# Kernel optimization log

Hardware: AMD Instinct MI355X
Metric: run time of the kernel (lower is better)

## Reference

```python
import jax, jax.numpy as jnp
import numpy as np

EPS = 1e-5
TAU = 2.0

# Heaviside spike with spikingjelly's default Sigmoid surrogate gradient (alpha=4)
@jax.custom_vjp
def spike(x):
    return (x >= 0.0).astype(x.dtype)

def _spike_fwd(x):
    return (x >= 0.0).astype(x.dtype), x

def _spike_bwd(x, g):
    a = 4.0
    s = jax.nn.sigmoid(a * x)
    return (g * a * s * (1.0 - s),)

spike.defvjp(_spike_fwd, _spike_bwd)

def lif(x_seq, v_th, v_reset):
    """Multi-step LIF (decay_input=True, detach_reset=True). v_reset=None -> soft reset."""
    def step(v, x):
        if v_reset is None:
            v = v + (x - v) / TAU
        else:
            v = v + (x - (v - v_reset)) / TAU
        s = spike(v - v_th)
        sd = jax.lax.stop_gradient(s)  # detach_reset=True
        if v_reset is None:
            v = v - sd * v_th
        else:
            v = (1.0 - sd) * v + sd * v_reset
        return v, s
    _, s_seq = jax.lax.scan(step, jnp.zeros_like(x_seq[0]), x_seq)
    return s_seq

def conv2d(x, w, groups=1):
    return jax.lax.conv_general_dilated(x, w, (1, 1), 'VALID',
        dimension_numbers=('NCHW', 'OIHW', 'NCHW'), feature_group_count=groups)

def bn(x, p):
    # p: [4, C] = (weight, bias, running_mean, running_var); inference-mode BN
    w, b, m, v = p
    inv = w * jax.lax.rsqrt(v + EPS)
    return x * inv[None, :, None, None] + (b - m * inv)[None, :, None, None]

def bn_pad(x, p):
    # BNAndPadLayer(pad_pixels=1): BN then pad 1px border with the BN of zeros
    y = bn(x, p)
    w, b, m, v = p
    pv = (b - m * w * jax.lax.rsqrt(v + EPS))[None, :, None, None]
    y = jnp.pad(y, ((0, 0), (0, 0), (1, 1), (1, 1)))
    y = y.at[:, :, :1, :].set(pv)
    y = y.at[:, :, -1:, :].set(pv)
    y = y.at[:, :, :, :1].set(pv)
    y = y.at[:, :, :, -1:].set(pv)
    return y

def repconv(x, w1, bn1, dw, pw, bn2):
    y = conv2d(x, w1)                       # 1x1 in->in
    y = bn_pad(y, bn1)                      # BN + 1px pad
    y = conv2d(y, dw, groups=dw.shape[0])   # depthwise 3x3, valid
    y = conv2d(y, pw)                       # 1x1 in->out
    return bn(y, bn2)

def setup_inputs() -> dict:
    T, B, C, H, W = 4, 16, 384, 32, 32
    key = jax.random.key(0)
    ks = iter(jax.random.split(key, 32))
    def bn_params(c):
        k1, k2, k3, k4 = jax.random.split(next(ks), 4)
        return jnp.stack([
            1.0 + 0.1 * jax.random.normal(k1, (c,)),
            0.1 * jax.random.normal(k2, (c,)),
            0.1 * jax.random.normal(k3, (c,)),
            jax.random.uniform(k4, (c,), minval=0.5, maxval=1.5)]).astype(jnp.float32)
    def conv_w(shape, fan_in):
        return (jax.random.normal(next(ks), shape) / np.sqrt(fan_in)).astype(jnp.float32)
    return dict(
        x=jax.random.normal(next(ks), (T, B, C, H, W), dtype=jnp.float32),
        r1_w1=conv_w((C, C, 1, 1), C),
        r1_bn1=bn_params(C),
        r1_dw=conv_w((C, 1, 3, 3), 9),
        r1_pw=conv_w((2 * C, C, 1, 1), C),
        r1_bn2=bn_params(2 * C),
        qkv_bn=bn_params(2 * C),
        r2_w1=conv_w((C, C, 1, 1), C),
        r2_bn1=bn_params(C),
        r2_dw=conv_w((C, 1, 3, 3), 9),
        r2_pw=conv_w((C, C, 1, 1), C),
        r2_bn2=bn_params(C),
        proj_bn=bn_params(C),
        scale=jnp.array([0.1], dtype=jnp.float32),
    )

def reference(x, r1_w1, r1_bn1, r1_dw, r1_pw, r1_bn2, qkv_bn,
              r2_w1, r2_bn1, r2_dw, r2_pw, r2_bn2, proj_bn, scale):
    T, B, C, H, W = x.shape
    xs = lif(x, 1.0, 0.0)                                  # shortcut_lif (hard reset)
    y = repconv(xs.reshape(T * B, C, H, W), r1_w1, r1_bn1, r1_dw, r1_pw, r1_bn2)
    y = bn(y, qkv_bn).reshape(T, B, 2 * C, H, W)           # qkv_conv outer BN
    qk, v = y[:, :, :C], y[:, :, C:]
    qk = lif(qk, 1.0, None)                                # qk_lif (soft reset)
    qk = qk.sum(axis=(-1, -2), keepdims=True)              # jit_sum over H,W -> [T,B,C,1,1]
    qk = lif(qk, 0.5, 0.0)                                 # talking_heads_lif (th=0.5, hard)
    v = lif(v, 1.0, None)                                  # v_lif (soft reset)
    out = qk * v                                           # jit_mul broadcast over H,W
    out = repconv(out.reshape(T * B, C, H, W), r2_w1, r2_bn1, r2_dw, r2_pw, r2_bn2)
    out = bn(out, proj_bn).reshape(T, B, C, H, W)          # proj_conv outer BN
    out = lif(out, 1.0, None)                              # proj_lif (soft reset)
    return out * scale
```

## Files before the change

kernel.cpp:

```cpp
#include <hip/hip_runtime.h>

typedef _Float16 f16;
typedef __attribute__((ext_vector_type(8))) _Float16 f16x8;
typedef __attribute__((ext_vector_type(4))) float f32x4;

#define TT 4
#define BB 16
#define CC 384

__device__ __forceinline__ float lif_soft(float x, float& v) {
  v = __fadd_rn(v, __fmul_rn(__fsub_rn(x, v), 0.5f));
  float s = (__fsub_rn(v, 1.0f) >= 0.0f) ? 1.0f : 0.0f;
  v = __fsub_rn(v, s);
  return s;
}
__device__ __forceinline__ float lif_hard(float x, float& v, float vth) {
  v = __fadd_rn(v, __fmul_rn(__fsub_rn(x, v), 0.5f));
  float s = (__fsub_rn(v, vth) >= 0.0f) ? 1.0f : 0.0f;
  if (s != 0.0f) v = 0.0f;
  return s;
}

__global__ __launch_bounds__(768) void k_prep(const float* __restrict__ bn1,
                                              const float* __restrict__ bn2,
                                              const float* __restrict__ qkv,
                                              const float* __restrict__ rbn1,
                                              const float* __restrict__ rbn2,
                                              const float* __restrict__ proj,
                                              float* __restrict__ par) {
  int c = threadIdx.x;
  float* s1 = par;          float* o1 = par + 384;
  float* sA = par + 768;    float* oA = par + 1536;
  float* s2 = par + 2304;   float* o2 = par + 2688;
  float* sB = par + 3072;   float* oB = par + 3456;
  if (c < 384) {
    double a = (double)bn1[c] / sqrt((double)bn1[3*384+c] + 1e-5);
    s1[c] = (float)a;
    o1[c] = (float)((double)bn1[384+c] - (double)bn1[2*384+c]*a);
    double a2 = (double)rbn1[c] / sqrt((double)rbn1[3*384+c] + 1e-5);
    s2[c] = (float)a2;
    o2[c] = (float)((double)rbn1[384+c] - (double)rbn1[2*384+c]*a2);
    double a3 = (double)rbn2[c] / sqrt((double)rbn2[3*384+c] + 1e-5);
    double b3 = (double)rbn2[384+c] - (double)rbn2[2*384+c]*a3;
    double a4 = (double)proj[c] / sqrt((double)proj[3*384+c] + 1e-5);
    double b4 = (double)proj[384+c] - (double)proj[2*384+c]*a4;
    sB[c] = (float)(a3*a4);
    oB[c] = (float)(b3*a4 + b4);
  }
  if (c < 768) {
    double a5 = (double)bn2[c] / sqrt((double)bn2[3*768+c] + 1e-5);
    double b5 = (double)bn2[768+c] - (double)bn2[2*768+c]*a5;
    double a6 = (double)qkv[c] / sqrt((double)qkv[3*768+c] + 1e-5);
    double b6 = (double)qkv[768+c] - (double)qkv[2*768+c]*a6;
    sA[c] = (float)(a5*a6);
    oA[c] = (float)(b5*a6 + b6);
  }
}

__global__ __launch_bounds__(256) void k_wsplit(const float* __restrict__ w,
                                                f16* __restrict__ wa, f16* __restrict__ wb, int n) {
  int i = blockIdx.x * 256 + threadIdx.x;
  if (i < n) {
    float x = w[i];
    f16 a = (f16)x;
    wa[i] = a;
    wb[i] = (f16)((x - (float)a) * 2048.0f);
  }
}

__global__ __launch_bounds__(256) void k_lif_in(const float* __restrict__ x, f16* __restrict__ xs) {
  __shared__ float tile[64][65];
  const int p0 = blockIdx.x * 64, c0 = blockIdx.y * 64, b = blockIdx.z;
  const int l = threadIdx.x & 63, q = threadIdx.x >> 6;
  float v[16];
  #pragma unroll
  for (int j = 0; j < 16; ++j) v[j] = 0.0f;
  for (int t = 0; t < TT; ++t) {
    __syncthreads();
    #pragma unroll
    for (int j = 0; j < 16; ++j) {
      int ci = q + j*4;
      tile[ci][l] = x[(((size_t)(t*BB + b)*CC + c0 + ci) << 10) + p0 + l];
    }
    __syncthreads();
    #pragma unroll
    for (int j = 0; j < 16; ++j) {
      int pi = q + j*4;
      float s = lif_hard(tile[l][pi], v[j], 1.0f);
      xs[((size_t)(t*BB + b)*1024 + p0 + pi)*CC + c0 + l] = (f16)s;
    }
  }
}

template<int EPI>
__device__ __forceinline__ void stage_arrT(const f16* __restrict__ g, int m0, int b_, int p0,
                                           int k0, f16* dst, int lane, int i0, int i1, bool isX) {
  #pragma unroll
  for (int i = i0; i < i1; ++i) {
    int loff = i*1024 + lane*16;
    int row = loff >> 6, col = loff & 63;
    int scol = col ^ (((row >> 1) & 3) << 4);
    int gm;
    if (EPI == 1 && isX) gm = ((row >> 5) << 14) + (b_ << 10) + p0 + (row & 31);
    else                 gm = m0 + row;
    const char* src = (const char*)g + (size_t)gm*768 + (size_t)(k0*2) + scol;
    __builtin_amdgcn_global_load_lds((const __attribute__((address_space(1))) void*)src,
                                     (__attribute__((address_space(3))) void*)((char*)dst + i*1024),
                                     16, 0, 0);
  }
}

__device__ __forceinline__ f16x8 fragld32(const f16* arr, int row, int fq) {
  int off = row*64 + ((fq*16) ^ (((row >> 1) & 3) << 4));
  return *(const f16x8*)((const char*)arr + off);
}

template<int NP, int EPI, int GATE>
__global__ __launch_bounds__(256, 2) void k_gemm(const f16* __restrict__ X1, const f16* __restrict__ X2,
    const f16* __restrict__ Wa, const f16* __restrict__ Wb,
    const float* __restrict__ scale, const float* __restrict__ bias,
    float* __restrict__ out0, float* __restrict__ out1,
    const f16* __restrict__ gatep, f16* __restrict__ sOut, f16* __restrict__ part) {
  constexpr int ARR = (NP == 3) ? 4 : 3;
  __shared__ __align__(16) f16 lds[2*ARR*4096];
  const int gx = gridDim.x;
  const int bid = blockIdx.y * gx + blockIdx.x;
  const int chunk = (gx * gridDim.y) >> 3;
  const int nb = (bid & 7) * chunk + (bid >> 3);
  const int o0 = (nb % gx) * 128;
  const int mb = nb / gx;
  const int m0 = mb * 128;
  const int b_ = mb >> 5, p0 = (mb & 31) << 5;
  const int lane = threadIdx.x & 63, wid = threadIdx.x >> 6;
  const int wr = wid >> 1, wc = wid & 1;
  const int fr = lane & 15, fq = lane >> 4;
  f32x4 acc_h[4][4], acc_l[4][4];
  #pragma unroll
  for (int i = 0; i < 4; ++i)
    #pragma unroll
    for (int j = 0; j < 4; ++j) { acc_h[i][j] = (f32x4){0,0,0,0}; acc_l[i][j] = (f32x4){0,0,0,0}; }

  auto stage_all = [&](int buf, int k0) {
    f16* base = lds + buf*(ARR*4096);
    if (NP == 3) {
      if (wid == 0)      stage_arrT<EPI>(X1, m0, b_, p0, k0, base,          lane, 0, 8, true);
      else if (wid == 1) stage_arrT<EPI>(X2, m0, b_, p0, k0, base + 4096,   lane, 0, 8, true);
      else if (wid == 2) stage_arrT<EPI>(Wa, o0, b_, p0, k0, base + 2*4096, lane, 0, 8, false);
      else               stage_arrT<EPI>(Wb, o0, b_, p0, k0, base + 3*4096, lane, 0, 8, false);
    } else {
      if (wid == 0)      stage_arrT<EPI>(X1, m0, b_, p0, k0, base,          lane, 0, 4, true);
      else if (wid == 1) stage_arrT<EPI>(X1, m0, b_, p0, k0, base,          lane, 4, 8, true);
      else if (wid == 2) stage_arrT<EPI>(Wa, o0, b_, p0, k0, base + 4096,   lane, 0, 8, false);
      else               stage_arrT<EPI>(Wb, o0, b_, p0, k0, base + 2*4096, lane, 0, 8, false);
    }
  };

  const char* gbase = nullptr;
  f16x8 g8{}, gn{};
  if constexpr (GATE) {
    gbase = (const char*)gatep + (size_t)(m0 >> 10)*768 + fq*16;
    g8 = *(const f16x8*)gbase;
  }

  stage_all(0, 0);
  __syncthreads();

  for (int it = 0; it < 12; ++it) {
    const int cur = it & 1;
    if (it < 11) stage_all(cur ^ 1, (it + 1)*32);
    if constexpr (GATE) { if (it < 11) gn = *(const f16x8*)(gbase + (it + 1)*64); }
    const f16* bX1 = lds + cur*(ARR*4096);
    const f16* bW1 = (NP == 3) ? bX1 + 2*4096 : bX1 + 4096;
    const f16* bW2 = (NP == 3) ? bX1 + 3*4096 : bX1 + 2*4096;
    f16x8 a1[4], b1[4], b2[4];
    #pragma unroll
    for (int mi = 0; mi < 4; ++mi) a1[mi] = fragld32(bX1, wr*64 + mi*16 + fr, fq);
    if constexpr (GATE) {
      #pragma unroll
      for (int mi = 0; mi < 4; ++mi) a1[mi] = a1[mi] * g8;
    }
    #pragma unroll
    for (int oi = 0; oi < 4; ++oi) {
      b1[oi] = fragld32(bW1, wc*64 + oi*16 + fr, fq);
      b2[oi] = fragld32(bW2, wc*64 + oi*16 + fr, fq);
    }
    if (NP == 3) {
      const f16* bX2 = bX1 + 4096;
      f16x8 a2[4];
      #pragma unroll
      for (int mi = 0; mi < 4; ++mi) a2[mi] = fragld32(bX2, wr*64 + mi*16 + fr, fq);
      #pragma unroll
      for (int mi = 0; mi < 4; ++mi)
        #pragma unroll
        for (int oi = 0; oi < 4; ++oi) {
          acc_h[mi][oi] = __builtin_amdgcn_mfma_f32_16x16x32_f16(a1[mi], b1[oi], acc_h[mi][oi], 0, 0, 0);
          acc_l[mi][oi] = __builtin_amdgcn_mfma_f32_16x16x32_f16(a1[mi], b2[oi], acc_l[mi][oi], 0, 0, 0);
          acc_l[mi][oi] = __builtin_amdgcn_mfma_f32_16x16x32_f16(a2[mi], b1[oi], acc_l[mi][oi], 0, 0, 0);
        }
    } else {
      #pragma unroll
      for (int mi = 0; mi < 4; ++mi)
        #pragma unroll
        for (int oi = 0; oi < 4; ++oi) {
          acc_h[mi][oi] = __builtin_amdgcn_mfma_f32_16x16x32_f16(a1[mi], b1[oi], acc_h[mi][oi], 0, 0, 0);
          acc_l[mi][oi] = __builtin_amdgcn_mfma_f32_16x16x32_f16(a1[mi], b2[oi], acc_l[mi][oi], 0, 0, 0);
        }
    }
    __syncthreads();
    if constexpr (GATE) { if (it < 11) g8 = gn; }
  }

  if constexpr (EPI == 0) {
    #pragma unroll
    for (int oi = 0; oi < 4; ++oi) {
      int o = o0 + wc*64 + oi*16 + fr;
      float sc = scale[o], bi = bias[o];
      float* op = out0; int oc = o;
      if (o >= 384) { op = out1; oc = o - 384; }
      #pragma unroll
      for (int mi = 0; mi < 4; ++mi) {
        f32x4 h = acc_h[mi][oi], lo2 = acc_l[mi][oi];
        #pragma unroll
        for (int r = 0; r < 4; ++r) {
          int m = m0 + wr*64 + mi*16 + fq*4 + r;
          float y = fmaf(0.00048828125f, lo2[r], h[r]);
          op[(size_t)m*384 + oc] = fmaf(y, sc, bi);
        }
      }
    }
  } else {
    float* T = (float*)lds;
    #pragma unroll
    for (int oi = 0; oi < 4; ++oi) {
      int ol = wc*64 + oi*16 + fr;
      float sc = scale[o0 + ol], bi = bias[o0 + ol];
      #pragma unroll
      for (int mi = 0; mi < 4; ++mi) {
        f32x4 h = acc_h[mi][oi], lo2 = acc_l[mi][oi];
        #pragma unroll
        for (int r = 0; r < 4; ++r) {
          int R = wr*64 + mi*16 + fq*4 + r;
          float y = fmaf(0.00048828125f, lo2[r], h[r]);
          T[R*128 + ol] = fmaf(y, sc, bi);
        }
      }
    }
    __syncthreads();
    const int tid = threadIdx.x;
    const int oc = tid & 127, ph = tid >> 7;
    if (o0 >= 384) {
      const int ocg = (o0 - 384) + oc;
      #pragma unroll
      for (int i = 0; i < 16; ++i) {
        int p = ph*16 + i;
        float v = 0.0f;
        #pragma unroll
        for (int t = 0; t < TT; ++t) {
          float s = lif_soft(T[(t*32 + p)*128 + oc], v);
          sOut[((size_t)((t*16 + b_)*1024 + p0 + p))*384 + ocg] = (f16)s;
        }
      }
    } else {
      float ps4[4] = {0,0,0,0};
      for (int i = 0; i < 16; ++i) {
        int p = ph*16 + i;
        float v = 0.0f;
        #pragma unroll
        for (int t = 0; t < TT; ++t) ps4[t] += lif_soft(T[(t*32 + p)*128 + oc], v);
      }
      int slice = (p0 >> 4) + ph;
      #pragma unroll
      for (int t = 0; t < TT; ++t)
        part[(((size_t)slice*4 + t)*16 + b_)*384 + o0 + oc] = (f16)ps4[t];
    }
  }
}

__global__ __launch_bounds__(256) void k_dw(const float* __restrict__ in, const float* __restrict__ wd,
                                            const float* __restrict__ pv,
                                            f16* __restrict__ outA, f16* __restrict__ outB) {
  const int ct = blockIdx.x, h = blockIdx.y, n = blockIdx.z;
  const int c = ct*64 + (threadIdx.x & 63);
  const int wq = threadIdx.x >> 6;
  float w9[9];
  #pragma unroll
  for (int i = 0; i < 9; ++i) w9[i] = wd[c*9 + i];
  const float pvc = pv[c];
  const float* base = in + (size_t)n*1024*CC;
  for (int wi = 0; wi < 8; ++wi) {
    int w = wq*8 + wi;
    float acc = 0.0f;
    #pragma unroll
    for (int dh = -1; dh <= 1; ++dh)
      #pragma unroll
      for (int dw = -1; dw <= 1; ++dw) {
        int hh = h + dh, ww = w + dw;
        float vv = ((unsigned)hh < 32u && (unsigned)ww < 32u) ? base[(size_t)(hh*32 + ww)*CC + c] : pvc;
        acc = fmaf(w9[(dh+1)*3 + dw + 1], vv, acc);
      }
    f16 a = (f16)acc;
    size_t off = ((size_t)n*1024 + h*32 + w)*CC + c;
    outA[off] = a;
    outB[off] = (f16)((acc - (float)a) * 2048.0f);
  }
}

__global__ __launch_bounds__(256) void k_gate(const f16* __restrict__ partial, f16* __restrict__ gate16) {
  int g = blockIdx.x*256 + threadIdx.x;
  int b = g / CC, c = g % CC;
  float sums[4];
  #pragma unroll
  for (int t = 0; t < TT; ++t) {
    float s = 0.0f;
    for (int ps = 0; ps < 64; ++ps) s += (float)partial[(((size_t)ps*4 + t)*BB + b)*CC + c];
    sums[t] = s;
  }
  float v = 0.0f;
  #pragma unroll
  for (int t = 0; t < TT; ++t)
    gate16[((size_t)(t*BB + b))*CC + c] = (f16)lif_hard(sums[t], v, 0.5f);
}

__global__ __launch_bounds__(256) void k_lif_out(const float* __restrict__ z, const float* __restrict__ scalep,
                                                 float* __restrict__ out) {
  __shared__ float tile[64][65];
  const int p0 = blockIdx.x * 64, c0 = blockIdx.y * 64, b = blockIdx.z;
  const int l = threadIdx.x & 63, q = threadIdx.x >> 6;
  const float sc = scalep[0];
  float v[16];
  #pragma unroll
  for (int j = 0; j < 16; ++j) v[j] = 0.0f;
  for (int t = 0; t < TT; ++t) {
    __syncthreads();
    #pragma unroll
    for (int j = 0; j < 16; ++j) {
      int pi = q + j*4;
      tile[pi][l] = z[((size_t)(t*BB + b)*1024 + p0 + pi)*CC + c0 + l];
    }
    __syncthreads();
    #pragma unroll
    for (int j = 0; j < 16; ++j) {
      int ci = q + j*4;
      float s = lif_soft(tile[l][ci], v[j]) * sc;
      out[(((size_t)(t*BB + b))*CC + c0 + ci)*1024 + p0 + l] = s;
    }
  }
}

extern "C" void kernel_launch(void* const* d_in, const int* in_sizes, int n_in,
                              void* d_out, int out_size, void* d_ws, size_t ws_size,
                              hipStream_t stream) {
  const float* x      = (const float*)d_in[0];
  const float* r1_w1  = (const float*)d_in[1];
  const float* r1_bn1 = (const float*)d_in[2];
  const float* r1_dw  = (const float*)d_in[3];
  const float* r1_pw  = (const float*)d_in[4];
  const float* r1_bn2 = (const float*)d_in[5];
  const float* qkv_bn = (const float*)d_in[6];
  const float* r2_w1  = (const float*)d_in[7];
  const float* r2_bn1 = (const float*)d_in[8];
  const float* r2_dw  = (const float*)d_in[9];
  const float* r2_pw  = (const float*)d_in[10];
  const float* r2_bn2 = (const float*)d_in[11];
  const float* proj_bn= (const float*)d_in[12];
  const float* scale  = (const float*)d_in[13];

  float* ws = (float*)d_ws;
  const size_t SEG = 12582912;
  float* W0f = ws;
  float* W1  = ws + SEG;
  float* W2f = ws + 3*SEG;
  float* W3  = ws + 4*SEG;
  f16* xs  = (f16*)W0f;
  f16* p1a = (f16*)W0f;
  f16* p2b = (f16*)W0f;
  f16* p1b = (f16*)W2f;
  f16* p2a = (f16*)W2f;
  float* t1  = W1;
  f16*  s16  = (f16*)W1;
  float* z   = W1;
  float* t2  = W3;

  f16* wsp = (f16*)(ws + 6*SEG);
  f16* w1a = wsp,              *w1b = wsp + 147456;
  f16* pwa = wsp + 294912,     *pwb = wsp + 589824;
  f16* q1a = wsp + 884736,     *q1b = wsp + 1032192;
  f16* qpa = wsp + 1179648,    *qpb = wsp + 1327104;
  f16* partial = wsp + 1474560;
  f16* gate16  = wsp + 3047424;
  float* par = (float*)(wsp + 3072000);
  float* s1 = par,        *o1 = par + 384;
  float* sA = par + 768,  *oA = par + 1536;
  float* s2 = par + 2304, *o2 = par + 2688;
  float* sB = par + 3072, *oB = par + 3456;

  const f16* nf = (const f16*)nullptr;
  f16* nf2 = (f16*)nullptr;

  k_prep<<<1, 768, 0, stream>>>(r1_bn1, r1_bn2, qkv_bn, r2_bn1, r2_bn2, proj_bn, par);
  k_wsplit<<<576, 256, 0, stream>>>(r1_w1, w1a, w1b, 147456);
  k_wsplit<<<1152, 256, 0, stream>>>(r1_pw, pwa, pwb, 294912);
  k_wsplit<<<576, 256, 0, stream>>>(r2_w1, q1a, q1b, 147456);
  k_wsplit<<<576, 256, 0, stream>>>(r2_pw, qpa, qpb, 147456);
  k_lif_in<<<dim3(16, 6, 16), 256, 0, stream>>>(x, xs);
  k_gemm<2,0,0><<<dim3(3, 512), 256, 0, stream>>>(xs, nf, w1a, w1b, s1, o1, t1, t1, nf, nf2, nf2);
  k_dw<<<dim3(6, 32, 64), 256, 0, stream>>>(t1, r1_dw, o1, p1a, p1b);
  k_gemm<3,1,0><<<dim3(6, 512), 256, 0, stream>>>(p1a, p1b, pwa, pwb, sA, oA,
                                                  (float*)nullptr, (float*)nullptr, nf, s16, partial);
  k_gate<<<24, 256, 0, stream>>>(partial, gate16);
  k_gemm<2,0,1><<<dim3(3, 512), 256, 0, stream>>>(s16, nf, q1a, q1b, s2, o2, t2, t2, gate16, nf2, nf2);
  k_dw<<<dim3(6, 32, 64), 256, 0, stream>>>(t2, r2_dw, o2, p2a, p2b);
  k_gemm<3,0,0><<<dim3(3, 512), 256, 0, stream>>>(p2a, p2b, qpa, qpb, sB, oB, z, z, nf, nf2, nf2);
  k_lif_out<<<dim3(16, 6, 16), 256, 0, stream>>>(z, scale, (float*)d_out);
}
```

Measured before the change: 544.3 us.

## Fuse final proj LIF and NCHW transpose into last GEMM epilogue

Adds an EPI==2 epilogue to the last pointwise GEMM. It gathers the time-major rows (as EPI 1 does), stages the BN output in LDS, runs the proj soft-reset LIF over T, scales the result and writes NCHW output directly. This removes the fp32 z round trip and the separate k_lif_out transpose kernel. It also XOR-swizzles the LDS staging tile to reduce bank conflicts and unrolls the depthwise loop. The cost is a reordered M tiling for that GEMM and strided stores along the pixel dimension in the epilogue.

Result: faster. 519.1 us (-4.6%).

```diff
diff --git a/kernel.cpp b/kernel.cpp
--- a/kernel.cpp
+++ b/kernel.cpp
@@ -101,7 +101,7 @@
     int row = loff >> 6, col = loff & 63;
     int scol = col ^ (((row >> 1) & 3) << 4);
     int gm;
-    if (EPI == 1 && isX) gm = ((row >> 5) << 14) + (b_ << 10) + p0 + (row & 31);
+    if (EPI >= 1 && isX) gm = ((row >> 5) << 14) + (b_ << 10) + p0 + (row & 31);
     else                 gm = m0 + row;
     const char* src = (const char*)g + (size_t)gm*768 + (size_t)(k0*2) + scol;
     __builtin_amdgcn_global_load_lds((const __attribute__((address_space(1))) void*)src,
@@ -119,7 +119,7 @@
 __global__ __launch_bounds__(256, 2) void k_gemm(const f16* __restrict__ X1, const f16* __restrict__ X2,
     const f16* __restrict__ Wa, const f16* __restrict__ Wb,
     const float* __restrict__ scale, const float* __restrict__ bias,
-    float* __restrict__ out0, float* __restrict__ out1,
+    float* __restrict__ out0, const float* __restrict__ out1,
     const f16* __restrict__ gatep, f16* __restrict__ sOut, f16* __restrict__ part) {
   constexpr int ARR = (NP == 3) ? 4 : 3;
   __shared__ __align__(16) f16 lds[2*ARR*4096];
@@ -215,8 +215,6 @@
     for (int oi = 0; oi < 4; ++oi) {
       int o = o0 + wc*64 + oi*16 + fr;
       float sc = scale[o], bi = bias[o];
-      float* op = out0; int oc = o;
-      if (o >= 384) { op = out1; oc = o - 384; }
       #pragma unroll
       for (int mi = 0; mi < 4; ++mi) {
         f32x4 h = acc_h[mi][oi], lo2 = acc_l[mi][oi];
@@ -224,7 +222,7 @@
         for (int r = 0; r < 4; ++r) {
           int m = m0 + wr*64 + mi*16 + fq*4 + r;
           float y = fmaf(0.00048828125f, lo2[r], h[r]);
-          op[(size_t)m*384 + oc] = fmaf(y, sc, bi);
+          out0[(size_t)m*384 + o] = fmaf(y, sc, bi);
         }
       }
     }
@@ -241,37 +239,57 @@
         for (int r = 0; r < 4; ++r) {
           int R = wr*64 + mi*16 + fq*4 + r;
           float y = fmaf(0.00048828125f, lo2[r], h[r]);
-          T[R*128 + ol] = fmaf(y, sc, bi);
+          T[R*128 + (ol ^ (R & 31))] = fmaf(y, sc, bi);
         }
       }
     }
     __syncthreads();
     const int tid = threadIdx.x;
-    const int oc = tid & 127, ph = tid >> 7;
-    if (o0 >= 384) {
-      const int ocg = (o0 - 384) + oc;
-      #pragma unroll
-      for (int i = 0; i < 16; ++i) {
-        int p = ph*16 + i;
-        float v = 0.0f;
-        #pragma unroll
-        for (int t = 0; t < TT; ++t) {
-          float s = lif_soft(T[(t*32 + p)*128 + oc], v);
-          sOut[((size_t)((t*16 + b_)*1024 + p0 + p))*384 + ocg] = (f16)s;
-        }
+    if constexpr (EPI == 1) {
+      const int oc = tid & 127, ph = tid >> 7;
+      if (o0 >= 384) {
+        const int ocg = (o0 - 384) + oc;
+        #pragma unroll
+        for (int i = 0; i < 16; ++i) {
+          int p = ph*16 + i;
+          float v = 0.0f;
+          #pragma unroll
+          for (int t = 0; t < TT; ++t) {
+            int R = t*32 + p;
+            float s = lif_soft(T[R*128 + (oc ^ (R & 31))], v);
+            sOut[((size_t)((t*16 + b_)*1024 + p0 + p))*384 + ocg] = (f16)s;
+          }
+        }
+      } else {
+        float ps4[4] = {0,0,0,0};
+        for (int i = 0; i < 16; ++i) {
+          int p = ph*16 + i;
+          float v = 0.0f;
+          #pragma unroll
+          for (int t = 0; t < TT; ++t) {
+            int R = t*32 + p;
+            ps4[t] += lif_soft(T[R*128 + (oc ^ (R & 31))], v);
+          }
+        }
+        int slice = (p0 >> 4) + ph;
+        #pragma unroll
+        for (int t = 0; t < TT; ++t)
+          part[(((size_t)slice*4 + t)*16 + b_)*384 + o0 + oc] = (f16)ps4[t];
       }
     } else {
-      float ps4[4] = {0,0,0,0};
-      for (int i = 0; i < 16; ++i) {
-        int p = ph*16 + i;
+      const int p = tid & 31, cg = tid >> 5;
+      const float gsc = out1[0];
+      #pragma unroll
+      for (int j = 0; j < 16; ++j) {
+        int c = cg*16 + j;
         float v = 0.0f;
         #pragma unroll
-        for (int t = 0; t < TT; ++t) ps4[t] += lif_soft(T[(t*32 + p)*128 + oc], v);
+        for (int t = 0; t < TT; ++t) {
+          int R = t*32 + p;
+          float s = lif_soft(T[R*128 + (c ^ (R & 31))], v) * gsc;
+          out0[(((size_t)(t*16 + b_)*384) + o0 + c)*1024 + p0 + p] = s;
+        }
       }
-      int slice = (p0 >> 4) + ph;
-      #pragma unroll
-      for (int t = 0; t < TT; ++t)
-        part[(((size_t)slice*4 + t)*16 + b_)*384 + o0 + oc] = (f16)ps4[t];
     }
   }
 }
@@ -287,6 +305,7 @@
   for (int i = 0; i < 9; ++i) w9[i] = wd[c*9 + i];
   const float pvc = pv[c];
   const float* base = in + (size_t)n*1024*CC;
+  #pragma unroll
   for (int wi = 0; wi < 8; ++wi) {
     int w = wq*8 + wi;
     float acc = 0.0f;
@@ -319,32 +338,6 @@
   #pragma unroll
   for (int t = 0; t < TT; ++t)
     gate16[((size_t)(t*BB + b))*CC + c] = (f16)lif_hard(sums[t], v, 0.5f);
-}
-
-__global__ __launch_bounds__(256) void k_lif_out(const float* __restrict__ z, const float* __restrict__ scalep,
-                                                 float* __restrict__ out) {
-  __shared__ float tile[64][65];
-  const int p0 = blockIdx.x * 64, c0 = blockIdx.y * 64, b = blockIdx.z;
-  const int l = threadIdx.x & 63, q = threadIdx.x >> 6;
-  const float sc = scalep[0];
-  float v[16];
-  #pragma unroll
-  for (int j = 0; j < 16; ++j) v[j] = 0.0f;
-  for (int t = 0; t < TT; ++t) {
-    __syncthreads();
-    #pragma unroll
-    for (int j = 0; j < 16; ++j) {
-      int pi = q + j*4;
-      tile[pi][l] = z[((size_t)(t*BB + b)*1024 + p0 + pi)*CC + c0 + l];
-    }
-    __syncthreads();
-    #pragma unroll
-    for (int j = 0; j < 16; ++j) {
-      int ci = q + j*4;
-      float s = lif_soft(tile[l][ci], v[j]) * sc;
-      out[(((size_t)(t*BB + b))*CC + c0 + ci)*1024 + p0 + l] = s;
-    }
-  }
 }
 
 extern "C" void kernel_launch(void* const* d_in, const int* in_sizes, int n_in,
@@ -378,7 +371,6 @@
   f16* p2a = (f16*)W2f;
   float* t1  = W1;
   f16*  s16  = (f16*)W1;
-  float* z   = W1;
   float* t2  = W3;
 
   f16* wsp = (f16*)(ws + 6*SEG);
@@ -403,13 +395,13 @@
   k_wsplit<<<576, 256, 0, stream>>>(r2_w1, q1a, q1b, 147456);
   k_wsplit<<<576, 256, 0, stream>>>(r2_pw, qpa, qpb, 147456);
   k_lif_in<<<dim3(16, 6, 16), 256, 0, stream>>>(x, xs);
-  k_gemm<2,0,0><<<dim3(3, 512), 256, 0, stream>>>(xs, nf, w1a, w1b, s1, o1, t1, t1, nf, nf2, nf2);
+  k_gemm<2,0,0><<<dim3(3, 512), 256, 0, stream>>>(xs, nf, w1a, w1b, s1, o1, t1, nullptr, nf, nf2, nf2);
   k_dw<<<dim3(6, 32, 64), 256, 0, stream>>>(t1, r1_dw, o1, p1a, p1b);
   k_gemm<3,1,0><<<dim3(6, 512), 256, 0, stream>>>(p1a, p1b, pwa, pwb, sA, oA,
-                                                  (float*)nullptr, (float*)nullptr, nf, s16, partial);
+                                                  nullptr, nullptr, nf, s16, partial);
   k_gate<<<24, 256, 0, stream>>>(partial, gate16);
-  k_gemm<2,0,1><<<dim3(3, 512), 256, 0, stream>>>(s16, nf, q1a, q1b, s2, o2, t2, t2, gate16, nf2, nf2);
+  k_gemm<2,0,1><<<dim3(3, 512), 256, 0, stream>>>(s16, nf, q1a, q1b, s2, o2, t2, nullptr, gate16, nf2, nf2);
   k_dw<<<dim3(6, 32, 64), 256, 0, stream>>>(t2, r2_dw, o2, p2a, p2b);
-  k_gemm<3,0,0><<<dim3(3, 512), 256, 0, stream>>>(p2a, p2b, qpa, qpb, sB, oB, z, z, nf, nf2, nf2);
-  k_lif_out<<<dim3(16, 6, 16), 256, 0, stream>>>(z, scale, (float*)d_out);
-}
+  k_gemm<3,2,0><<<dim3(3, 512), 256, 0, stream>>>(p2a, p2b, qpa, qpb, sB, oB,
+                                                  (float*)d_out, scale, nf, nf2, nf2);
+}
```
